# Kernel tuning notes

Measured on AMD Instinct MI355X. Metric: run time of the kernel, lower is better.

## Reference

```python
import jax, jax.numpy as jnp
import numpy as np

B, S, H = 1, 1024, 2880
NQ, NKV, D = 64, 8, 64          # query heads, kv heads, head_dim
G = NQ // NKV                    # GQA group size
W = 128                          # sliding window
SCALE = D ** -0.5
NEG = -1e30


def rotate_half(x):
    x1, x2 = jnp.split(x, 2, axis=-1)
    return jnp.concatenate((-x2, x1), axis=-1)


def setup_inputs() -> dict:
    key = jax.random.key(0)
    ks = jax.random.split(key, 8)
    hidden_states = jax.random.normal(ks[0], (B, S, H), jnp.float32)
    # rotary tables, half head_dim (module concats (cos,cos) to full dim)
    pos = jnp.arange(S, dtype=jnp.float32)[:, None]
    inv = 1.0 / (10000.0 ** (jnp.arange(0, D, 2, dtype=jnp.float32) / D))
    ang = pos * inv[None, :]                      # (S, D/2)
    cos = jnp.cos(ang)[None].astype(jnp.float32)  # (1, S, D/2)
    sin = jnp.sin(ang)[None].astype(jnp.float32)
    w_qkv = jax.random.normal(ks[1], (H, (NQ + 2 * NKV) * D), jnp.float32) * 0.02
    b_qkv = jax.random.normal(ks[2], ((NQ + 2 * NKV) * D,), jnp.float32) * 0.02
    w_o = jax.random.normal(ks[3], (NQ * D, H), jnp.float32) * 0.02
    b_o = jax.random.normal(ks[4], (H,), jnp.float32) * 0.02
    sinks = jax.random.normal(ks[5], (NQ,), jnp.float32)
    k_cache = jnp.zeros((B, S, NKV, D), jnp.float32)
    v_cache = jnp.zeros((B, S, NKV, D), jnp.float32)
    return {"hidden_states": hidden_states, "cos": cos, "sin": sin,
            "w_qkv": w_qkv, "b_qkv": b_qkv, "w_o": w_o, "b_o": b_o,
            "sinks": sinks, "k_cache": k_cache, "v_cache": v_cache, "kv_len": 0}


def reference(hidden_states, cos, sin, w_qkv, b_qkv, w_o, b_o, sinks,
              k_cache, v_cache, kv_len):
    # fused QKV projection + split
    qkv = hidden_states @ w_qkv + b_qkv                      # (B, S, (NQ+2*NKV)*D)
    q, k, v = jnp.split(qkv, [NQ * D, NQ * D + NKV * D], axis=-1)
    q = q.reshape(B, S, NQ, D)
    k = k.reshape(B, S, NKV, D)
    v = v.reshape(B, S, NKV, D)
    # RoPE (BSND layout, half-dim tables duplicated to full dim)
    cosf = jnp.concatenate((cos, cos), axis=-1)[:, :, None, :]
    sinf = jnp.concatenate((sin, sin), axis=-1)[:, :, None, :]
    q = q * cosf + rotate_half(q) * sinf
    k = k * cosf + rotate_half(k) * sinf
    # KV-cache scatter update at position kv_len along seq dim
    k_cache = jax.lax.dynamic_update_slice(k_cache, k, (0, kv_len, 0, 0))
    v_cache = jax.lax.dynamic_update_slice(v_cache, v, (0, kv_len, 0, 0))
    T = kv_len + S
    keys = k_cache[:, :T]                                    # (B, T, NKV, D)
    vals = v_cache[:, :T]
    # GQA: group query heads by kv head
    qg = q.reshape(B, S, NKV, G, D)
    scores = jnp.einsum('bqhgd,bkhd->bhgqk', qg, keys) * SCALE  # (B,NKV,G,S,T)
    # causal + sliding-window mask
    i = jnp.arange(S)[:, None] + kv_len
    j = jnp.arange(T)[None, :]
    allowed = (j <= i) & (i - j < W)
    scores = jnp.where(allowed, scores, NEG)
    # softmax with per-head learnable sink logit (sink gets no value)
    sk = sinks.reshape(NKV, G)[None, :, :, None]             # (1,NKV,G,1)
    m = jnp.maximum(jnp.max(scores, axis=-1), sk)            # (B,NKV,G,S)
    p = jnp.exp(scores - m[..., None])
    denom = jnp.sum(p, axis=-1) + jnp.exp(sk - m)
    attn = jnp.einsum('bhgqk,bkhd->bqhgd', p / denom[..., None], vals)
    out = attn.reshape(B, S, NQ * D) @ w_o + b_o             # (B, S, H)
    return out
```

## Files before the change

kernel.cpp:

```cpp
#include <hip/hip_runtime.h>
#include <hip/hip_bf16.h>

#define NQH 64
#define NKVH 8
#define DH 64
#define SEQ 1024
#define HID 2880
#define QKV_N 5120
#define ATTN_N 4096
#define WIN 128
#define WO_NPAD 2944
#define SCALE_F 0.125f

typedef __attribute__((ext_vector_type(8))) __bf16 bf16x8;
typedef __attribute__((ext_vector_type(4))) float f32x4;

#define GLOAD_LDS16(g, l) \
    __builtin_amdgcn_global_load_lds((const __attribute__((address_space(1))) void*)(g), \
                                     (__attribute__((address_space(3))) void*)(l), 16, 0, 0)

__device__ __forceinline__ ushort f2bf(float x) {
    union { float f; unsigned int u; } c; c.f = x;
    unsigned int u = c.u;
    unsigned int r = (u + 0x7FFFu + ((u >> 16) & 1u)) >> 16;
    return (ushort)r;
}

__global__ __launch_bounds__(256) void convert_f32_bf16(
    const float* __restrict__ in, ushort* __restrict__ out, int n4)
{
    int idx = blockIdx.x * blockDim.x + threadIdx.x;
    int stride = gridDim.x * blockDim.x;
    for (int i = idx; i < n4; i += stride) {
        float4 v = reinterpret_cast<const float4*>(in)[i];
        ushort4 o;
        o.x = f2bf(v.x); o.y = f2bf(v.y); o.z = f2bf(v.z); o.w = f2bf(v.w);
        reinterpret_cast<ushort4*>(out)[i] = o;
    }
}

__global__ __launch_bounds__(256) void transpose_convert(
    const float* __restrict__ in, ushort* __restrict__ out, int K, int N)
{
    __shared__ ushort tile[64][80];
    const int bk = blockIdx.x * 64;
    const int bn = blockIdx.y * 64;
    const int tid = threadIdx.x;
    const bool inb = bn < N;

#pragma unroll
    for (int it = 0; it < 4; ++it) {
        int r = it * 16 + (tid >> 4);
        int c4 = (tid & 15) * 4;
        float4 v = make_float4(0.f, 0.f, 0.f, 0.f);
        if (inb) v = *(const float4*)&in[(size_t)(bk + r) * N + bn + c4];
        tile[c4 + 0][r] = f2bf(v.x);
        tile[c4 + 1][r] = f2bf(v.y);
        tile[c4 + 2][r] = f2bf(v.z);
        tile[c4 + 3][r] = f2bf(v.w);
    }
    __syncthreads();
#pragma unroll
    for (int it = 0; it < 2; ++it) {
        int nr = it * 32 + (tid >> 3);
        int c8 = (tid & 7) * 8;
        uint4 v = *(const uint4*)&tile[nr][c8];
        *(uint4*)&out[(size_t)(bn + nr) * K + bk + c8] = v;
    }
}

template<bool ROPE>
__global__ __launch_bounds__(256) void gemm64x128(
    const ushort* __restrict__ A, const ushort* __restrict__ BT,
    const float* __restrict__ bias, float* __restrict__ C,
    int K, int ldC, int Nreal,
    const float* __restrict__ cosp, const float* __restrict__ sinp)
{
    __shared__ ushort Al[2 * 64 * 64];
    __shared__ ushort Bl[2 * 128 * 64];
    const int t = threadIdx.x;
    const int lane = t & 63;
    const int w = t >> 6;
    const int wr = w >> 1, wc = w & 1;
    const int g4 = lane >> 4;
    const int r15 = lane & 15;

    const int flat = blockIdx.x + gridDim.x * blockIdx.y;
    const int per = (gridDim.x * gridDim.y) >> 3;
    const int virt = (flat & 7) * per + (flat >> 3);
    const int m0 = (virt & 15) * 64;
    const int n0 = (virt >> 4) * 128;

    const ushort* aSrc0; const ushort* aSrc1;
    ushort* aDst0; ushort* aDst1;
    {
        int lin0 = t, lin1 = 256 + t;
        int row0 = lin0 >> 3, row1 = lin1 >> 3;
        int ch0 = (lin0 & 7) ^ (row0 & 7);
        int ch1 = (lin1 & 7) ^ (row1 & 7);
        aSrc0 = A + (size_t)(m0 + row0) * K + ch0 * 8;
        aSrc1 = A + (size_t)(m0 + row1) * K + ch1 * 8;
        aDst0 = &Al[lin0 * 8];
        aDst1 = &Al[lin1 * 8];
    }
    const ushort* bSrc0; const ushort* bSrc1; const ushort* bSrc2; const ushort* bSrc3;
    ushort* bDst0; ushort* bDst1; ushort* bDst2; ushort* bDst3;
    {
        int lin;
        lin = t;       bSrc0 = BT + (size_t)(n0 + (lin >> 3)) * K + (((lin & 7) ^ ((lin >> 3) & 7)) * 8); bDst0 = &Bl[lin * 8];
        lin = 256 + t; bSrc1 = BT + (size_t)(n0 + (lin >> 3)) * K + (((lin & 7) ^ ((lin >> 3) & 7)) * 8); bDst1 = &Bl[lin * 8];
        lin = 512 + t; bSrc2 = BT + (size_t)(n0 + (lin >> 3)) * K + (((lin & 7) ^ ((lin >> 3) & 7)) * 8); bDst2 = &Bl[lin * 8];
        lin = 768 + t; bSrc3 = BT + (size_t)(n0 + (lin >> 3)) * K + (((lin & 7) ^ ((lin >> 3) & 7)) * 8); bDst3 = &Bl[lin * 8];
    }

#define STAGE_TILE(bufsel) do { \
        GLOAD_LDS16(aSrc0, aDst0 + (bufsel) * 4096); \
        GLOAD_LDS16(aSrc1, aDst1 + (bufsel) * 4096); \
        GLOAD_LDS16(bSrc0, bDst0 + (bufsel) * 8192); \
        GLOAD_LDS16(bSrc1, bDst1 + (bufsel) * 8192); \
        GLOAD_LDS16(bSrc2, bDst2 + (bufsel) * 8192); \
        GLOAD_LDS16(bSrc3, bDst3 + (bufsel) * 8192); \
        aSrc0 += 64; aSrc1 += 64; \
        bSrc0 += 64; bSrc1 += 64; bSrc2 += 64; bSrc3 += 64; \
    } while (0)

    int aoff[2][2], boff[4][2];
#pragma unroll
    for (int mi = 0; mi < 2; ++mi)
#pragma unroll
        for (int ks = 0; ks < 2; ++ks) {
            int row = wr * 32 + mi * 16 + r15;
            int slot = (ks * 4 + g4) ^ (row & 7);
            aoff[mi][ks] = row * 64 + slot * 8;
        }
#pragma unroll
    for (int ni = 0; ni < 4; ++ni)
#pragma unroll
        for (int ks = 0; ks < 2; ++ks) {
            int col = wc * 64 + ni * 16 + r15;
            int slot = (ks * 4 + g4) ^ (col & 7);
            boff[ni][ks] = col * 64 + slot * 8;
        }

    f32x4 acc[2][4];
#pragma unroll
    for (int mi = 0; mi < 2; ++mi)
#pragma unroll
        for (int ni = 0; ni < 4; ++ni) acc[mi][ni] = (f32x4){0.f, 0.f, 0.f, 0.f};

#define COMPUTE_TILE(bufsel) do { \
        const ushort* Ab = &Al[(bufsel) * 4096]; \
        const ushort* Bb = &Bl[(bufsel) * 8192]; \
        _Pragma("unroll") \
        for (int ks = 0; ks < 2; ++ks) { \
            bf16x8 a0 = *(const bf16x8*)&Ab[aoff[0][ks]]; \
            bf16x8 a1 = *(const bf16x8*)&Ab[aoff[1][ks]]; \
            bf16x8 b0 = *(const bf16x8*)&Bb[boff[0][ks]]; \
            bf16x8 b1 = *(const bf16x8*)&Bb[boff[1][ks]]; \
            bf16x8 b2 = *(const bf16x8*)&Bb[boff[2][ks]]; \
            bf16x8 b3 = *(const bf16x8*)&Bb[boff[3][ks]]; \
            acc[0][0] = __builtin_amdgcn_mfma_f32_16x16x32_bf16(a0, b0, acc[0][0], 0, 0, 0); \
            acc[0][1] = __builtin_amdgcn_mfma_f32_16x16x32_bf16(a0, b1, acc[0][1], 0, 0, 0); \
            acc[0][2] = __builtin_amdgcn_mfma_f32_16x16x32_bf16(a0, b2, acc[0][2], 0, 0, 0); \
            acc[0][3] = __builtin_amdgcn_mfma_f32_16x16x32_bf16(a0, b3, acc[0][3], 0, 0, 0); \
            acc[1][0] = __builtin_amdgcn_mfma_f32_16x16x32_bf16(a1, b0, acc[1][0], 0, 0, 0); \
            acc[1][1] = __builtin_amdgcn_mfma_f32_16x16x32_bf16(a1, b1, acc[1][1], 0, 0, 0); \
            acc[1][2] = __builtin_amdgcn_mfma_f32_16x16x32_bf16(a1, b2, acc[1][2], 0, 0, 0); \
            acc[1][3] = __builtin_amdgcn_mfma_f32_16x16x32_bf16(a1, b3, acc[1][3], 0, 0, 0); \
        } \
    } while (0)

    const int NT = K >> 6;
    STAGE_TILE(0);
    __syncthreads();
    for (int kt = 0; kt < NT; kt += 2) {
        if (kt + 1 < NT) STAGE_TILE(1);
        COMPUTE_TILE(0);
        __syncthreads();
        if (kt + 1 < NT) {
            if (kt + 2 < NT) STAGE_TILE(0);
            COMPUTE_TILE(1);
            __syncthreads();
        }
    }
#undef STAGE_TILE
#undef COMPUTE_TILE

    float vals[2][4][4];
#pragma unroll
    for (int ni = 0; ni < 4; ++ni) {
        int col = n0 + wc * 64 + ni * 16 + r15;
        float bv = (col < Nreal) ? bias[col] : 0.f;
#pragma unroll
        for (int mi = 0; mi < 2; ++mi)
#pragma unroll
            for (int r = 0; r < 4; ++r) vals[mi][ni][r] = acc[mi][ni][r] + bv;
    }
    if (ROPE) {
        const int head = (n0 + wc * 64) >> 6;
        if (head < 72) {
#pragma unroll
            for (int mi = 0; mi < 2; ++mi)
#pragma unroll
                for (int r = 0; r < 4; ++r) {
                    int q = m0 + wr * 32 + mi * 16 + g4 * 4 + r;
#pragma unroll
                    for (int dp = 0; dp < 2; ++dp) {
                        int d = dp * 16 + r15;
                        float c = cosp[q * 32 + d];
                        float s = sinp[q * 32 + d];
                        float x1 = vals[mi][dp][r];
                        float x2 = vals[mi][dp + 2][r];
                        vals[mi][dp][r]     = x1 * c - x2 * s;
                        vals[mi][dp + 2][r] = x2 * c + x1 * s;
                    }
                }
        }
    }
#pragma unroll
    for (int ni = 0; ni < 4; ++ni) {
        int col = n0 + wc * 64 + ni * 16 + r15;
        if (col < Nreal) {
#pragma unroll
            for (int mi = 0; mi < 2; ++mi) {
                int row = m0 + wr * 32 + mi * 16 + g4 * 4;
#pragma unroll
                for (int r = 0; r < 4; ++r)
                    C[(size_t)(row + r) * ldC + col] = vals[mi][ni][r];
            }
        }
    }
}

__global__ __launch_bounds__(512) void attn_mfma_kernel(
    const float* __restrict__ qkv, const float* __restrict__ sinks,
    ushort* __restrict__ attn_out)
{
    __shared__ __align__(16) ushort Kl[160][72];
    __shared__ __align__(16) ushort Vt[64][168];
    __shared__ __align__(16) ushort Pl[8][32][40];
    const int t = threadIdx.x;
    const int w = t >> 6;
    const int l = t & 63;
    const int g4 = l >> 4;
    const int r15 = l & 15;
    const int q0 = blockIdx.x * 32;
    const int hk = blockIdx.y;
    const int kbase = q0 - 128;

#pragma unroll
    for (int i = 0; i < 5; ++i) {
        int idx = i * 512 + t;
        int row = idx >> 4;
        int c4 = (idx & 15) * 4;
        int j = kbase + row;
        float4 kv = make_float4(0.f, 0.f, 0.f, 0.f);
        float4 vv = make_float4(0.f, 0.f, 0.f, 0.f);
        if (j >= 0) {
            kv = *(const float4*)&qkv[(size_t)j * QKV_N + 4096 + hk * 64 + c4];
            vv = *(const float4*)&qkv[(size_t)j * QKV_N + 4608 + hk * 64 + c4];
        }
        ushort4 kp;
        kp.x = f2bf(kv.x); kp.y = f2bf(kv.y); kp.z = f2bf(kv.z); kp.w = f2bf(kv.w);
        *(ushort4*)&Kl[row][c4] = kp;
        Vt[c4 + 0][row] = f2bf(vv.x);
        Vt[c4 + 1][row] = f2bf(vv.y);
        Vt[c4 + 2][row] = f2bf(vv.z);
        Vt[c4 + 3][row] = f2bf(vv.w);
    }

    bf16x8 qf[2][2];
#pragma unroll
    for (int ct = 0; ct < 2; ++ct) {
        int R = w * 32 + ct * 16 + r15;
        int q = q0 + (R & 31);
        int hq = hk * 8 + (R >> 5);
        const float* qb = &qkv[(size_t)q * QKV_N + hq * 64];
#pragma unroll
        for (int s = 0; s < 2; ++s) {
            float4 a = *(const float4*)&qb[s * 32 + g4 * 8];
            float4 b = *(const float4*)&qb[s * 32 + g4 * 8 + 4];
            union { ushort u[8]; bf16x8 v; } pk;
            pk.u[0] = f2bf(a.x * SCALE_F); pk.u[1] = f2bf(a.y * SCALE_F);
            pk.u[2] = f2bf(a.z * SCALE_F); pk.u[3] = f2bf(a.w * SCALE_F);
            pk.u[4] = f2bf(b.x * SCALE_F); pk.u[5] = f2bf(b.y * SCALE_F);
            pk.u[6] = f2bf(b.z * SCALE_F); pk.u[7] = f2bf(b.w * SCALE_F);
            qf[ct][s] = pk.v;
        }
    }
    __syncthreads();

    f32x4 sc[10][2];
#pragma unroll
    for (int kt = 0; kt < 10; ++kt) {
        sc[kt][0] = (f32x4){0.f, 0.f, 0.f, 0.f};
        sc[kt][1] = (f32x4){0.f, 0.f, 0.f, 0.f};
    }
#pragma unroll
    for (int kt = 0; kt < 10; ++kt) {
#pragma unroll
        for (int s = 0; s < 2; ++s) {
            bf16x8 kf = *(const bf16x8*)&Kl[kt * 16 + r15][s * 32 + g4 * 8];
            sc[kt][0] = __builtin_amdgcn_mfma_f32_16x16x32_bf16(kf, qf[0][s], sc[kt][0], 0, 0, 0);
            sc[kt][1] = __builtin_amdgcn_mfma_f32_16x16x32_bf16(kf, qf[1][s], sc[kt][1], 0, 0, 0);
        }
    }

    const int minkey = 128 - q0;
#pragma unroll
    for (int ct = 0; ct < 2; ++ct) {
        int R = w * 32 + ct * 16 + r15;
        int ql = R & 31;
        float snk = sinks[hk * 8 + (R >> 5)];
#pragma unroll
        for (int kt = 0; kt < 10; ++kt)
#pragma unroll
            for (int r = 0; r < 4; ++r) {
                int key = kt * 16 + g4 * 4 + r;
                bool ok = (key > ql) && (key <= ql + 128) && (key >= minkey);
                if (!ok) sc[kt][ct][r] = -1e30f;
            }
        float m = snk;
#pragma unroll
        for (int kt = 0; kt < 10; ++kt)
#pragma unroll
            for (int r = 0; r < 4; ++r) m = fmaxf(m, sc[kt][ct][r]);
        m = fmaxf(m, __shfl_xor(m, 16));
        m = fmaxf(m, __shfl_xor(m, 32));
        float sum = 0.f;
#pragma unroll
        for (int kt = 0; kt < 10; ++kt)
#pragma unroll
            for (int r = 0; r < 4; ++r) {
                float p = __expf(sc[kt][ct][r] - m);
                sc[kt][ct][r] = p;
                sum += p;
            }
        sum += __shfl_xor(sum, 16);
        sum += __shfl_xor(sum, 32);
        sum += __expf(snk - m);
        float iv = 1.0f / sum;
#pragma unroll
        for (int kt = 0; kt < 10; ++kt)
#pragma unroll
            for (int r = 0; r < 4; ++r) sc[kt][ct][r] *= iv;
    }

    f32x4 pv[2][4];
#pragma unroll
    for (int mi = 0; mi < 2; ++mi)
#pragma unroll
        for (int ni = 0; ni < 4; ++ni) pv[mi][ni] = (f32x4){0.f, 0.f, 0.f, 0.f};

#pragma unroll
    for (int s = 0; s < 5; ++s) {
#pragma unroll
        for (int ct = 0; ct < 2; ++ct)
#pragma unroll
            for (int kh = 0; kh < 2; ++kh) {
                int kt = 2 * s + kh;
                ushort4 p4;
                p4.x = f2bf(sc[kt][ct][0]);
                p4.y = f2bf(sc[kt][ct][1]);
                p4.z = f2bf(sc[kt][ct][2]);
                p4.w = f2bf(sc[kt][ct][3]);
                *(ushort4*)&Pl[w][ct * 16 + r15][kh * 16 + g4 * 4] = p4;
            }
#pragma unroll
        for (int mi = 0; mi < 2; ++mi) {
            bf16x8 pf = *(const bf16x8*)&Pl[w][mi * 16 + r15][g4 * 8];
#pragma unroll
            for (int ni = 0; ni < 4; ++ni) {
                bf16x8 vf = *(const bf16x8*)&Vt[ni * 16 + r15][s * 32 + g4 * 8];
                pv[mi][ni] = __builtin_amdgcn_mfma_f32_16x16x32_bf16(pf, vf, pv[mi][ni], 0, 0, 0);
            }
        }
    }

#pragma unroll
    for (int mi = 0; mi < 2; ++mi)
#pragma unroll
        for (int r = 0; r < 4; ++r) {
            int R = w * 32 + mi * 16 + g4 * 4 + r;
            int q = q0 + (R & 31);
            int hq = hk * 8 + (R >> 5);
            ushort* ob = &attn_out[(size_t)q * ATTN_N + hq * 64 + r15];
#pragma unroll
            for (int ni = 0; ni < 4; ++ni)
                ob[ni * 16] = f2bf(pv[mi][ni][r]);
        }
}

extern "C" void kernel_launch(void* const* d_in, const int* in_sizes, int n_in,
                              void* d_out, int out_size, void* d_ws, size_t ws_size,
                              hipStream_t stream)
{
    const float* hidden = (const float*)d_in[0];
    const float* cosp   = (const float*)d_in[1];
    const float* sinp   = (const float*)d_in[2];
    const float* w_qkv  = (const float*)d_in[3];
    const float* b_qkv  = (const float*)d_in[4];
    const float* w_o    = (const float*)d_in[5];
    const float* b_o    = (const float*)d_in[6];
    const float* sinks  = (const float*)d_in[7];

    char* ws = (char*)d_ws;
    size_t off = 0;
    ushort* wqkvT = (ushort*)(ws + off); off += (size_t)QKV_N * HID * 2;
    ushort* woT   = (ushort*)(ws + off); off += (size_t)WO_NPAD * ATTN_N * 2;
    float*  qkv   = (float*)(ws + off);  off += (size_t)SEQ * QKV_N * 4;
    ushort* hidden_b = (ushort*)(ws + off);
    ushort* attn_b   = (ushort*)(ws + off); off += (size_t)SEQ * ATTN_N * 2;
    if (off > ws_size) return;

    transpose_convert<<<dim3(HID / 64, QKV_N / 64), 256, 0, stream>>>(w_qkv, wqkvT, HID, QKV_N);
    transpose_convert<<<dim3(ATTN_N / 64, WO_NPAD / 64), 256, 0, stream>>>(w_o, woT, ATTN_N, HID);
    convert_f32_bf16<<<2048, 256, 0, stream>>>(hidden, hidden_b, SEQ * HID / 4);

    gemm64x128<true><<<dim3(QKV_N / 128, SEQ / 64), 256, 0, stream>>>(
        hidden_b, wqkvT, b_qkv, qkv, HID, QKV_N, QKV_N, cosp, sinp);

    attn_mfma_kernel<<<dim3(SEQ / 32, NKVH), 512, 0, stream>>>(qkv, sinks, attn_b);

    gemm64x128<false><<<dim3(WO_NPAD / 128, SEQ / 64), 256, 0, stream>>>(
        attn_b, woT, b_o, (float*)d_out, ATTN_N, HID, HID, nullptr, nullptr);
}
```

Before: 147.9 us.

## Shrink GEMM tiles to 64x64 with triple-buffered LDS pipeline and MFMA priority

Replaces the 64x128 GEMM tile with a 64x64 tile, where each wave computes 16 rows by 64 columns. The grid doubles, which gives better occupancy and wave balance across CUs. The double-buffered LDS pipeline becomes a three-stage ring, with explicit vmcnt waits and raw s_barrier so that two tiles of global loads stay in flight. MFMA groups are also wrapped in s_setprio. The cost is less data reuse per block, more global/L2 traffic for the B operand, and reliance on exact vmcnt accounting.

```diff
diff --git a/kernel.cpp b/kernel.cpp
--- a/kernel.cpp
+++ b/kernel.cpp
@@ -70,18 +70,17 @@
 }
 
 template<bool ROPE>
-__global__ __launch_bounds__(256) void gemm64x128(
+__global__ __launch_bounds__(256) void gemm64x64(
     const ushort* __restrict__ A, const ushort* __restrict__ BT,
     const float* __restrict__ bias, float* __restrict__ C,
     int K, int ldC, int Nreal,
     const float* __restrict__ cosp, const float* __restrict__ sinp)
 {
-    __shared__ ushort Al[2 * 64 * 64];
-    __shared__ ushort Bl[2 * 128 * 64];
+    __shared__ ushort Al[3 * 4096];
+    __shared__ ushort Bl[3 * 4096];
     const int t = threadIdx.x;
     const int lane = t & 63;
     const int w = t >> 6;
-    const int wr = w >> 1, wc = w & 1;
     const int g4 = lane >> 4;
     const int r15 = lane & 15;
 
@@ -89,145 +88,124 @@
     const int per = (gridDim.x * gridDim.y) >> 3;
     const int virt = (flat & 7) * per + (flat >> 3);
     const int m0 = (virt & 15) * 64;
-    const int n0 = (virt >> 4) * 128;
-
-    const ushort* aSrc0; const ushort* aSrc1;
-    ushort* aDst0; ushort* aDst1;
+    const int n0 = (virt >> 4) * 64;
+
+    const ushort *aS0, *aS1, *bS0, *bS1;
+    int aO0, aO1;
     {
         int lin0 = t, lin1 = 256 + t;
         int row0 = lin0 >> 3, row1 = lin1 >> 3;
-        int ch0 = (lin0 & 7) ^ (row0 & 7);
-        int ch1 = (lin1 & 7) ^ (row1 & 7);
-        aSrc0 = A + (size_t)(m0 + row0) * K + ch0 * 8;
-        aSrc1 = A + (size_t)(m0 + row1) * K + ch1 * 8;
-        aDst0 = &Al[lin0 * 8];
-        aDst1 = &Al[lin1 * 8];
-    }
-    const ushort* bSrc0; const ushort* bSrc1; const ushort* bSrc2; const ushort* bSrc3;
-    ushort* bDst0; ushort* bDst1; ushort* bDst2; ushort* bDst3;
-    {
-        int lin;
-        lin = t;       bSrc0 = BT + (size_t)(n0 + (lin >> 3)) * K + (((lin & 7) ^ ((lin >> 3) & 7)) * 8); bDst0 = &Bl[lin * 8];
-        lin = 256 + t; bSrc1 = BT + (size_t)(n0 + (lin >> 3)) * K + (((lin & 7) ^ ((lin >> 3) & 7)) * 8); bDst1 = &Bl[lin * 8];
-        lin = 512 + t; bSrc2 = BT + (size_t)(n0 + (lin >> 3)) * K + (((lin & 7) ^ ((lin >> 3) & 7)) * 8); bDst2 = &Bl[lin * 8];
-        lin = 768 + t; bSrc3 = BT + (size_t)(n0 + (lin >> 3)) * K + (((lin & 7) ^ ((lin >> 3) & 7)) * 8); bDst3 = &Bl[lin * 8];
-    }
-
-#define STAGE_TILE(bufsel) do { \
-        GLOAD_LDS16(aSrc0, aDst0 + (bufsel) * 4096); \
-        GLOAD_LDS16(aSrc1, aDst1 + (bufsel) * 4096); \
-        GLOAD_LDS16(bSrc0, bDst0 + (bufsel) * 8192); \
-        GLOAD_LDS16(bSrc1, bDst1 + (bufsel) * 8192); \
-        GLOAD_LDS16(bSrc2, bDst2 + (bufsel) * 8192); \
-        GLOAD_LDS16(bSrc3, bDst3 + (bufsel) * 8192); \
-        aSrc0 += 64; aSrc1 += 64; \
-        bSrc0 += 64; bSrc1 += 64; bSrc2 += 64; bSrc3 += 64; \
+        int sl0 = (lin0 & 7) ^ (row0 & 7);
+        int sl1 = (lin1 & 7) ^ (row1 & 7);
+        aS0 = A  + (size_t)(m0 + row0) * K + sl0 * 8;
+        aS1 = A  + (size_t)(m0 + row1) * K + sl1 * 8;
+        bS0 = BT + (size_t)(n0 + row0) * K + sl0 * 8;
+        bS1 = BT + (size_t)(n0 + row1) * K + sl1 * 8;
+        aO0 = lin0 * 8; aO1 = lin1 * 8;
+    }
+
+#define STAGE_TILE(bi) do { \
+        GLOAD_LDS16(aS0, &Al[(bi) * 4096 + aO0]); \
+        GLOAD_LDS16(aS1, &Al[(bi) * 4096 + aO1]); \
+        GLOAD_LDS16(bS0, &Bl[(bi) * 4096 + aO0]); \
+        GLOAD_LDS16(bS1, &Bl[(bi) * 4096 + aO1]); \
+        aS0 += 64; aS1 += 64; bS0 += 64; bS1 += 64; \
     } while (0)
 
-    int aoff[2][2], boff[4][2];
-#pragma unroll
-    for (int mi = 0; mi < 2; ++mi)
-#pragma unroll
-        for (int ks = 0; ks < 2; ++ks) {
-            int row = wr * 32 + mi * 16 + r15;
-            int slot = (ks * 4 + g4) ^ (row & 7);
-            aoff[mi][ks] = row * 64 + slot * 8;
-        }
-#pragma unroll
-    for (int ni = 0; ni < 4; ++ni)
-#pragma unroll
-        for (int ks = 0; ks < 2; ++ks) {
-            int col = wc * 64 + ni * 16 + r15;
-            int slot = (ks * 4 + g4) ^ (col & 7);
-            boff[ni][ks] = col * 64 + slot * 8;
-        }
-
-    f32x4 acc[2][4];
-#pragma unroll
-    for (int mi = 0; mi < 2; ++mi)
-#pragma unroll
-        for (int ni = 0; ni < 4; ++ni) acc[mi][ni] = (f32x4){0.f, 0.f, 0.f, 0.f};
-
-#define COMPUTE_TILE(bufsel) do { \
-        const ushort* Ab = &Al[(bufsel) * 4096]; \
-        const ushort* Bb = &Bl[(bufsel) * 8192]; \
+    int aoff[2], boff[4][2];
+#pragma unroll
+    for (int ks = 0; ks < 2; ++ks) {
+        int row = w * 16 + r15;
+        aoff[ks] = row * 64 + (((ks * 4 + g4) ^ (row & 7)) * 8);
+#pragma unroll
+        for (int ni = 0; ni < 4; ++ni) {
+            int col = ni * 16 + r15;
+            boff[ni][ks] = col * 64 + (((ks * 4 + g4) ^ (col & 7)) * 8);
+        }
+    }
+
+    f32x4 acc[4];
+#pragma unroll
+    for (int ni = 0; ni < 4; ++ni) acc[ni] = (f32x4){0.f, 0.f, 0.f, 0.f};
+
+#define COMPUTE_TILE(bi) do { \
+        const ushort* Ab = &Al[(bi) * 4096]; \
+        const ushort* Bb = &Bl[(bi) * 4096]; \
         _Pragma("unroll") \
         for (int ks = 0; ks < 2; ++ks) { \
-            bf16x8 a0 = *(const bf16x8*)&Ab[aoff[0][ks]]; \
-            bf16x8 a1 = *(const bf16x8*)&Ab[aoff[1][ks]]; \
+            bf16x8 av = *(const bf16x8*)&Ab[aoff[ks]]; \
             bf16x8 b0 = *(const bf16x8*)&Bb[boff[0][ks]]; \
             bf16x8 b1 = *(const bf16x8*)&Bb[boff[1][ks]]; \
             bf16x8 b2 = *(const bf16x8*)&Bb[boff[2][ks]]; \
             bf16x8 b3 = *(const bf16x8*)&Bb[boff[3][ks]]; \
-            acc[0][0] = __builtin_amdgcn_mfma_f32_16x16x32_bf16(a0, b0, acc[0][0], 0, 0, 0); \
-            acc[0][1] = __builtin_amdgcn_mfma_f32_16x16x32_bf16(a0, b1, acc[0][1], 0, 0, 0); \
-            acc[0][2] = __builtin_amdgcn_mfma_f32_16x16x32_bf16(a0, b2, acc[0][2], 0, 0, 0); \
-            acc[0][3] = __builtin_amdgcn_mfma_f32_16x16x32_bf16(a0, b3, acc[0][3], 0, 0, 0); \
-            acc[1][0] = __builtin_amdgcn_mfma_f32_16x16x32_bf16(a1, b0, acc[1][0], 0, 0, 0); \
-            acc[1][1] = __builtin_amdgcn_mfma_f32_16x16x32_bf16(a1, b1, acc[1][1], 0, 0, 0); \
-            acc[1][2] = __builtin_amdgcn_mfma_f32_16x16x32_bf16(a1, b2, acc[1][2], 0, 0, 0); \
-            acc[1][3] = __builtin_amdgcn_mfma_f32_16x16x32_bf16(a1, b3, acc[1][3], 0, 0, 0); \
+            __builtin_amdgcn_s_setprio(1); \
+            acc[0] = __builtin_amdgcn_mfma_f32_16x16x32_bf16(av, b0, acc[0], 0, 0, 0); \
+            acc[1] = __builtin_amdgcn_mfma_f32_16x16x32_bf16(av, b1, acc[1], 0, 0, 0); \
+            acc[2] = __builtin_amdgcn_mfma_f32_16x16x32_bf16(av, b2, acc[2], 0, 0, 0); \
+            acc[3] = __builtin_amdgcn_mfma_f32_16x16x32_bf16(av, b3, acc[3], 0, 0, 0); \
+            __builtin_amdgcn_s_setprio(0); \
         } \
     } while (0)
 
     const int NT = K >> 6;
     STAGE_TILE(0);
-    __syncthreads();
-    for (int kt = 0; kt < NT; kt += 2) {
-        if (kt + 1 < NT) STAGE_TILE(1);
-        COMPUTE_TILE(0);
-        __syncthreads();
-        if (kt + 1 < NT) {
-            if (kt + 2 < NT) STAGE_TILE(0);
-            COMPUTE_TILE(1);
-            __syncthreads();
-        }
+    STAGE_TILE(1);
+    int bufC = 0, bufS = 2;
+    for (int kt = 0; kt < NT; ++kt) {
+        if (kt + 2 < NT) {
+            STAGE_TILE(bufS);
+            bufS = (bufS == 2) ? 0 : bufS + 1;
+            asm volatile("s_waitcnt vmcnt(8)" ::: "memory");
+        } else if (kt + 2 == NT) {
+            asm volatile("s_waitcnt vmcnt(4)" ::: "memory");
+        } else {
+            asm volatile("s_waitcnt vmcnt(0)" ::: "memory");
+        }
+        __builtin_amdgcn_s_barrier();
+        __builtin_amdgcn_sched_barrier(0);
+        COMPUTE_TILE(bufC);
+        bufC = (bufC == 2) ? 0 : bufC + 1;
+        __builtin_amdgcn_sched_barrier(0);
+        __builtin_amdgcn_s_barrier();
     }
 #undef STAGE_TILE
 #undef COMPUTE_TILE
 
-    float vals[2][4][4];
+    float vals[4][4];
 #pragma unroll
     for (int ni = 0; ni < 4; ++ni) {
-        int col = n0 + wc * 64 + ni * 16 + r15;
+        int col = n0 + ni * 16 + r15;
         float bv = (col < Nreal) ? bias[col] : 0.f;
 #pragma unroll
-        for (int mi = 0; mi < 2; ++mi)
-#pragma unroll
-            for (int r = 0; r < 4; ++r) vals[mi][ni][r] = acc[mi][ni][r] + bv;
+        for (int r = 0; r < 4; ++r) vals[ni][r] = acc[ni][r] + bv;
     }
     if (ROPE) {
-        const int head = (n0 + wc * 64) >> 6;
+        const int head = n0 >> 6;
         if (head < 72) {
 #pragma unroll
-            for (int mi = 0; mi < 2; ++mi)
-#pragma unroll
-                for (int r = 0; r < 4; ++r) {
-                    int q = m0 + wr * 32 + mi * 16 + g4 * 4 + r;
-#pragma unroll
-                    for (int dp = 0; dp < 2; ++dp) {
-                        int d = dp * 16 + r15;
-                        float c = cosp[q * 32 + d];
-                        float s = sinp[q * 32 + d];
-                        float x1 = vals[mi][dp][r];
-                        float x2 = vals[mi][dp + 2][r];
-                        vals[mi][dp][r]     = x1 * c - x2 * s;
-                        vals[mi][dp + 2][r] = x2 * c + x1 * s;
-                    }
+            for (int r = 0; r < 4; ++r) {
+                int q = m0 + w * 16 + g4 * 4 + r;
+#pragma unroll
+                for (int dp = 0; dp < 2; ++dp) {
+                    int d = dp * 16 + r15;
+                    float c = cosp[q * 32 + d];
+                    float s = sinp[q * 32 + d];
+                    float x1 = vals[dp][r];
+                    float x2 = vals[dp + 2][r];
+                    vals[dp][r]     = x1 * c - x2 * s;
+                    vals[dp + 2][r] = x2 * c + x1 * s;
                 }
+            }
         }
     }
 #pragma unroll
     for (int ni = 0; ni < 4; ++ni) {
-        int col = n0 + wc * 64 + ni * 16 + r15;
+        int col = n0 + ni * 16 + r15;
         if (col < Nreal) {
-#pragma unroll
-            for (int mi = 0; mi < 2; ++mi) {
-                int row = m0 + wr * 32 + mi * 16 + g4 * 4;
-#pragma unroll
-                for (int r = 0; r < 4; ++r)
-                    C[(size_t)(row + r) * ldC + col] = vals[mi][ni][r];
-            }
+            int row = m0 + w * 16 + g4 * 4;
+#pragma unroll
+            for (int r = 0; r < 4; ++r)
+                C[(size_t)(row + r) * ldC + col] = vals[ni][r];
         }
     }
 }
@@ -417,11 +395,11 @@
     transpose_convert<<<dim3(ATTN_N / 64, WO_NPAD / 64), 256, 0, stream>>>(w_o, woT, ATTN_N, HID);
     convert_f32_bf16<<<2048, 256, 0, stream>>>(hidden, hidden_b, SEQ * HID / 4);
 
-    gemm64x128<true><<<dim3(QKV_N / 128, SEQ / 64), 256, 0, stream>>>(
+    gemm64x64<true><<<dim3(QKV_N / 64, SEQ / 64), 256, 0, stream>>>(
         hidden_b, wqkvT, b_qkv, qkv, HID, QKV_N, QKV_N, cosp, sinp);
 
     attn_mfma_kernel<<<dim3(SEQ / 32, NKVH), 512, 0, stream>>>(qkv, sinks, attn_b);
 
-    gemm64x128<false><<<dim3(WO_NPAD / 128, SEQ / 64), 256, 0, stream>>>(
+    gemm64x64<false><<<dim3(WO_NPAD / 64, SEQ / 64), 256, 0, stream>>>(
         attn_b, woT, b_o, (float*)d_out, ATTN_N, HID, HID, nullptr, nullptr);
 }
```

Result: slower. 162.3 us (+9.7%).

## Split-K by two for QKV and output GEMMs with separate reduction kernel

Applied to the files above, without the earlier changes.

Both projection GEMMs now split the K dimension in two via blockIdx.z, doubling the block count. Each half writes fp32 partials to a workspace buffer, and a new elementwise kernel sums them. Bias is added only in the first split. RoPE is applied to each partial, which is valid because the rotation is linear. The K tile per stage is halved to 32 with a matching LDS swizzle, which improves wave coverage on the GPU but adds a large partial write/read round trip, two extra launches, and more barriers per unit of work.

```diff
diff --git a/kernel.cpp b/kernel.cpp
--- a/kernel.cpp
+++ b/kernel.cpp
@@ -39,6 +39,20 @@
     }
 }
 
+__global__ __launch_bounds__(256) void reduce_add(
+    const float4* __restrict__ a, const float4* __restrict__ b,
+    float4* __restrict__ o, int n4)
+{
+    int idx = blockIdx.x * blockDim.x + threadIdx.x;
+    int stride = gridDim.x * blockDim.x;
+    for (int i = idx; i < n4; i += stride) {
+        float4 x = a[i], y = b[i];
+        float4 r;
+        r.x = x.x + y.x; r.y = x.y + y.y; r.z = x.z + y.z; r.w = x.w + y.w;
+        o[i] = r;
+    }
+}
+
 __global__ __launch_bounds__(256) void transpose_convert(
     const float* __restrict__ in, ushort* __restrict__ out, int K, int N)
 {
@@ -70,20 +84,21 @@
 }
 
 template<bool ROPE>
-__global__ __launch_bounds__(256) void gemm64x128(
+__global__ __launch_bounds__(256) void gemm_sk(
     const ushort* __restrict__ A, const ushort* __restrict__ BT,
     const float* __restrict__ bias, float* __restrict__ C,
-    int K, int ldC, int Nreal,
+    int Khalf, int Kld, int ldC, int Nreal, size_t cstride,
     const float* __restrict__ cosp, const float* __restrict__ sinp)
 {
-    __shared__ ushort Al[2 * 64 * 64];
-    __shared__ ushort Bl[2 * 128 * 64];
+    __shared__ ushort Al[2 * 2048];
+    __shared__ ushort Bl[2 * 4096];
     const int t = threadIdx.x;
     const int lane = t & 63;
     const int w = t >> 6;
     const int wr = w >> 1, wc = w & 1;
     const int g4 = lane >> 4;
     const int r15 = lane & 15;
+    const int kz = blockIdx.z;
 
     const int flat = blockIdx.x + gridDim.x * blockIdx.y;
     const int per = (gridDim.x * gridDim.y) >> 3;
@@ -91,86 +106,67 @@
     const int m0 = (virt & 15) * 64;
     const int n0 = (virt >> 4) * 128;
 
-    const ushort* aSrc0; const ushort* aSrc1;
-    ushort* aDst0; ushort* aDst1;
+    const ushort *aS, *bS0, *bS1;
+    int aO, bO0, bO1;
     {
+        int rowA = t >> 2;
+        int chA = (t & 3) ^ ((rowA >> 1) & 3);
+        aS = A + (size_t)(m0 + rowA) * Kld + kz * Khalf + chA * 8;
+        aO = t * 8;
         int lin0 = t, lin1 = 256 + t;
-        int row0 = lin0 >> 3, row1 = lin1 >> 3;
-        int ch0 = (lin0 & 7) ^ (row0 & 7);
-        int ch1 = (lin1 & 7) ^ (row1 & 7);
-        aSrc0 = A + (size_t)(m0 + row0) * K + ch0 * 8;
-        aSrc1 = A + (size_t)(m0 + row1) * K + ch1 * 8;
-        aDst0 = &Al[lin0 * 8];
-        aDst1 = &Al[lin1 * 8];
-    }
-    const ushort* bSrc0; const ushort* bSrc1; const ushort* bSrc2; const ushort* bSrc3;
-    ushort* bDst0; ushort* bDst1; ushort* bDst2; ushort* bDst3;
-    {
-        int lin;
-        lin = t;       bSrc0 = BT + (size_t)(n0 + (lin >> 3)) * K + (((lin & 7) ^ ((lin >> 3) & 7)) * 8); bDst0 = &Bl[lin * 8];
-        lin = 256 + t; bSrc1 = BT + (size_t)(n0 + (lin >> 3)) * K + (((lin & 7) ^ ((lin >> 3) & 7)) * 8); bDst1 = &Bl[lin * 8];
-        lin = 512 + t; bSrc2 = BT + (size_t)(n0 + (lin >> 3)) * K + (((lin & 7) ^ ((lin >> 3) & 7)) * 8); bDst2 = &Bl[lin * 8];
-        lin = 768 + t; bSrc3 = BT + (size_t)(n0 + (lin >> 3)) * K + (((lin & 7) ^ ((lin >> 3) & 7)) * 8); bDst3 = &Bl[lin * 8];
-    }
-
-#define STAGE_TILE(bufsel) do { \
-        GLOAD_LDS16(aSrc0, aDst0 + (bufsel) * 4096); \
-        GLOAD_LDS16(aSrc1, aDst1 + (bufsel) * 4096); \
-        GLOAD_LDS16(bSrc0, bDst0 + (bufsel) * 8192); \
-        GLOAD_LDS16(bSrc1, bDst1 + (bufsel) * 8192); \
-        GLOAD_LDS16(bSrc2, bDst2 + (bufsel) * 8192); \
-        GLOAD_LDS16(bSrc3, bDst3 + (bufsel) * 8192); \
-        aSrc0 += 64; aSrc1 += 64; \
-        bSrc0 += 64; bSrc1 += 64; bSrc2 += 64; bSrc3 += 64; \
+        int rowB0 = lin0 >> 2, rowB1 = lin1 >> 2;
+        int chB0 = (lin0 & 3) ^ ((rowB0 >> 1) & 3);
+        int chB1 = (lin1 & 3) ^ ((rowB1 >> 1) & 3);
+        bS0 = BT + (size_t)(n0 + rowB0) * Kld + kz * Khalf + chB0 * 8;
+        bS1 = BT + (size_t)(n0 + rowB1) * Kld + kz * Khalf + chB1 * 8;
+        bO0 = lin0 * 8; bO1 = lin1 * 8;
+    }
+
+#define STAGE_TILE(buf) do { \
+        GLOAD_LDS16(aS,  &Al[(buf) * 2048 + aO]); \
+        GLOAD_LDS16(bS0, &Bl[(buf) * 4096 + bO0]); \
+        GLOAD_LDS16(bS1, &Bl[(buf) * 4096 + bO1]); \
+        aS += 32; bS0 += 32; bS1 += 32; \
     } while (0)
 
-    int aoff[2][2], boff[4][2];
+    int aoff[2], boff[4];
+#pragma unroll
+    for (int mi = 0; mi < 2; ++mi) {
+        int row = wr * 32 + mi * 16 + r15;
+        aoff[mi] = row * 32 + ((g4 ^ ((row >> 1) & 3)) * 8);
+    }
+#pragma unroll
+    for (int ni = 0; ni < 4; ++ni) {
+        int col = wc * 64 + ni * 16 + r15;
+        boff[ni] = col * 32 + ((g4 ^ ((col >> 1) & 3)) * 8);
+    }
+
+    f32x4 acc[2][4];
 #pragma unroll
     for (int mi = 0; mi < 2; ++mi)
 #pragma unroll
-        for (int ks = 0; ks < 2; ++ks) {
-            int row = wr * 32 + mi * 16 + r15;
-            int slot = (ks * 4 + g4) ^ (row & 7);
-            aoff[mi][ks] = row * 64 + slot * 8;
-        }
-#pragma unroll
-    for (int ni = 0; ni < 4; ++ni)
-#pragma unroll
-        for (int ks = 0; ks < 2; ++ks) {
-            int col = wc * 64 + ni * 16 + r15;
-            int slot = (ks * 4 + g4) ^ (col & 7);
-            boff[ni][ks] = col * 64 + slot * 8;
-        }
-
-    f32x4 acc[2][4];
-#pragma unroll
-    for (int mi = 0; mi < 2; ++mi)
-#pragma unroll
         for (int ni = 0; ni < 4; ++ni) acc[mi][ni] = (f32x4){0.f, 0.f, 0.f, 0.f};
 
-#define COMPUTE_TILE(bufsel) do { \
-        const ushort* Ab = &Al[(bufsel) * 4096]; \
-        const ushort* Bb = &Bl[(bufsel) * 8192]; \
-        _Pragma("unroll") \
-        for (int ks = 0; ks < 2; ++ks) { \
-            bf16x8 a0 = *(const bf16x8*)&Ab[aoff[0][ks]]; \
-            bf16x8 a1 = *(const bf16x8*)&Ab[aoff[1][ks]]; \
-            bf16x8 b0 = *(const bf16x8*)&Bb[boff[0][ks]]; \
-            bf16x8 b1 = *(const bf16x8*)&Bb[boff[1][ks]]; \
-            bf16x8 b2 = *(const bf16x8*)&Bb[boff[2][ks]]; \
-            bf16x8 b3 = *(const bf16x8*)&Bb[boff[3][ks]]; \
-            acc[0][0] = __builtin_amdgcn_mfma_f32_16x16x32_bf16(a0, b0, acc[0][0], 0, 0, 0); \
-            acc[0][1] = __builtin_amdgcn_mfma_f32_16x16x32_bf16(a0, b1, acc[0][1], 0, 0, 0); \
-            acc[0][2] = __builtin_amdgcn_mfma_f32_16x16x32_bf16(a0, b2, acc[0][2], 0, 0, 0); \
-            acc[0][3] = __builtin_amdgcn_mfma_f32_16x16x32_bf16(a0, b3, acc[0][3], 0, 0, 0); \
-            acc[1][0] = __builtin_amdgcn_mfma_f32_16x16x32_bf16(a1, b0, acc[1][0], 0, 0, 0); \
-            acc[1][1] = __builtin_amdgcn_mfma_f32_16x16x32_bf16(a1, b1, acc[1][1], 0, 0, 0); \
-            acc[1][2] = __builtin_amdgcn_mfma_f32_16x16x32_bf16(a1, b2, acc[1][2], 0, 0, 0); \
-            acc[1][3] = __builtin_amdgcn_mfma_f32_16x16x32_bf16(a1, b3, acc[1][3], 0, 0, 0); \
-        } \
+#define COMPUTE_TILE(buf) do { \
+        const ushort* Ab = &Al[(buf) * 2048]; \
+        const ushort* Bb = &Bl[(buf) * 4096]; \
+        bf16x8 a0 = *(const bf16x8*)&Ab[aoff[0]]; \
+        bf16x8 a1 = *(const bf16x8*)&Ab[aoff[1]]; \
+        bf16x8 b0 = *(const bf16x8*)&Bb[boff[0]]; \
+        bf16x8 b1 = *(const bf16x8*)&Bb[boff[1]]; \
+        bf16x8 b2 = *(const bf16x8*)&Bb[boff[2]]; \
+        bf16x8 b3 = *(const bf16x8*)&Bb[boff[3]]; \
+        acc[0][0] = __builtin_amdgcn_mfma_f32_16x16x32_bf16(a0, b0, acc[0][0], 0, 0, 0); \
+        acc[0][1] = __builtin_amdgcn_mfma_f32_16x16x32_bf16(a0, b1, acc[0][1], 0, 0, 0); \
+        acc[0][2] = __builtin_amdgcn_mfma_f32_16x16x32_bf16(a0, b2, acc[0][2], 0, 0, 0); \
+        acc[0][3] = __builtin_amdgcn_mfma_f32_16x16x32_bf16(a0, b3, acc[0][3], 0, 0, 0); \
+        acc[1][0] = __builtin_amdgcn_mfma_f32_16x16x32_bf16(a1, b0, acc[1][0], 0, 0, 0); \
+        acc[1][1] = __builtin_amdgcn_mfma_f32_16x16x32_bf16(a1, b1, acc[1][1], 0, 0, 0); \
+        acc[1][2] = __builtin_amdgcn_mfma_f32_16x16x32_bf16(a1, b2, acc[1][2], 0, 0, 0); \
+        acc[1][3] = __builtin_amdgcn_mfma_f32_16x16x32_bf16(a1, b3, acc[1][3], 0, 0, 0); \
     } while (0)
 
-    const int NT = K >> 6;
+    const int NT = Khalf >> 5;
     STAGE_TILE(0);
     __syncthreads();
     for (int kt = 0; kt < NT; kt += 2) {
@@ -190,7 +186,7 @@
 #pragma unroll
     for (int ni = 0; ni < 4; ++ni) {
         int col = n0 + wc * 64 + ni * 16 + r15;
-        float bv = (col < Nreal) ? bias[col] : 0.f;
+        float bv = (kz == 0 && col < Nreal) ? bias[col] : 0.f;
 #pragma unroll
         for (int mi = 0; mi < 2; ++mi)
 #pragma unroll
@@ -217,6 +213,7 @@
                 }
         }
     }
+    float* Cz = C + (size_t)kz * cstride;
 #pragma unroll
     for (int ni = 0; ni < 4; ++ni) {
         int col = n0 + wc * 64 + ni * 16 + r15;
@@ -226,7 +223,7 @@
                 int row = m0 + wr * 32 + mi * 16 + g4 * 4;
 #pragma unroll
                 for (int r = 0; r < 4; ++r)
-                    C[(size_t)(row + r) * ldC + col] = vals[mi][ni][r];
+                    Cz[(size_t)(row + r) * ldC + col] = vals[mi][ni][r];
             }
         }
     }
@@ -411,17 +408,26 @@
     float*  qkv   = (float*)(ws + off);  off += (size_t)SEQ * QKV_N * 4;
     ushort* hidden_b = (ushort*)(ws + off);
     ushort* attn_b   = (ushort*)(ws + off); off += (size_t)SEQ * ATTN_N * 2;
+    float*  part  = (float*)(ws + off);  off += (size_t)2 * SEQ * QKV_N * 4;
     if (off > ws_size) return;
 
     transpose_convert<<<dim3(HID / 64, QKV_N / 64), 256, 0, stream>>>(w_qkv, wqkvT, HID, QKV_N);
     transpose_convert<<<dim3(ATTN_N / 64, WO_NPAD / 64), 256, 0, stream>>>(w_o, woT, ATTN_N, HID);
     convert_f32_bf16<<<2048, 256, 0, stream>>>(hidden, hidden_b, SEQ * HID / 4);
 
-    gemm64x128<true><<<dim3(QKV_N / 128, SEQ / 64), 256, 0, stream>>>(
-        hidden_b, wqkvT, b_qkv, qkv, HID, QKV_N, QKV_N, cosp, sinp);
+    gemm_sk<true><<<dim3(QKV_N / 128, SEQ / 64, 2), 256, 0, stream>>>(
+        hidden_b, wqkvT, b_qkv, part, HID / 2, HID, QKV_N, QKV_N,
+        (size_t)SEQ * QKV_N, cosp, sinp);
+    reduce_add<<<2048, 256, 0, stream>>>(
+        (const float4*)part, (const float4*)(part + (size_t)SEQ * QKV_N),
+        (float4*)qkv, SEQ * QKV_N / 4);
 
     attn_mfma_kernel<<<dim3(SEQ / 32, NKVH), 512, 0, stream>>>(qkv, sinks, attn_b);
 
-    gemm64x128<false><<<dim3(WO_NPAD / 128, SEQ / 64), 256, 0, stream>>>(
-        attn_b, woT, b_o, (float*)d_out, ATTN_N, HID, HID, nullptr, nullptr);
-}
+    gemm_sk<false><<<dim3(WO_NPAD / 128, SEQ / 64, 2), 256, 0, stream>>>(
+        attn_b, woT, b_o, part, ATTN_N / 2, ATTN_N, HID, HID,
+        (size_t)SEQ * HID, nullptr, nullptr);
+    reduce_add<<<2048, 256, 0, stream>>>(
+        (const float4*)part, (const float4*)(part + (size_t)SEQ * HID),
+        (float4*)d_out, SEQ * HID / 4);
+}
```

Result: slower. 173.9 us (+17.5%).

## Enlarge GEMM block tile to 128x128 for both projections

Applied to the files above, without the earlier changes.

Both projection GEMMs now compute a 128x128 output tile per block instead of 64x128. Each wave runs a 4x4 grid of MFMA fragments, and each thread issues four A and four B async loads per k-step. The goal is more data reuse per LDS load and fewer global reads per flop. The cost is half as many blocks, which may leave CUs idle (the output projection has only 184 blocks), plus more LDS and accumulator registers per block.

```diff
diff --git a/kernel.cpp b/kernel.cpp
--- a/kernel.cpp
+++ b/kernel.cpp
@@ -70,14 +70,14 @@
 }
 
 template<bool ROPE>
-__global__ __launch_bounds__(256) void gemm64x128(
+__global__ __launch_bounds__(256) void gemm128sq(
     const ushort* __restrict__ A, const ushort* __restrict__ BT,
     const float* __restrict__ bias, float* __restrict__ C,
     int K, int ldC, int Nreal,
     const float* __restrict__ cosp, const float* __restrict__ sinp)
 {
-    __shared__ ushort Al[2 * 64 * 64];
-    __shared__ ushort Bl[2 * 128 * 64];
+    __shared__ ushort Al[2 * 8192];
+    __shared__ ushort Bl[2 * 8192];
     const int t = threadIdx.x;
     const int lane = t & 63;
     const int w = t >> 6;
@@ -88,85 +88,75 @@
     const int flat = blockIdx.x + gridDim.x * blockIdx.y;
     const int per = (gridDim.x * gridDim.y) >> 3;
     const int virt = (flat & 7) * per + (flat >> 3);
-    const int m0 = (virt & 15) * 64;
-    const int n0 = (virt >> 4) * 128;
-
-    const ushort* aSrc0; const ushort* aSrc1;
-    ushort* aDst0; ushort* aDst1;
-    {
-        int lin0 = t, lin1 = 256 + t;
-        int row0 = lin0 >> 3, row1 = lin1 >> 3;
-        int ch0 = (lin0 & 7) ^ (row0 & 7);
-        int ch1 = (lin1 & 7) ^ (row1 & 7);
-        aSrc0 = A + (size_t)(m0 + row0) * K + ch0 * 8;
-        aSrc1 = A + (size_t)(m0 + row1) * K + ch1 * 8;
-        aDst0 = &Al[lin0 * 8];
-        aDst1 = &Al[lin1 * 8];
-    }
-    const ushort* bSrc0; const ushort* bSrc1; const ushort* bSrc2; const ushort* bSrc3;
-    ushort* bDst0; ushort* bDst1; ushort* bDst2; ushort* bDst3;
-    {
-        int lin;
-        lin = t;       bSrc0 = BT + (size_t)(n0 + (lin >> 3)) * K + (((lin & 7) ^ ((lin >> 3) & 7)) * 8); bDst0 = &Bl[lin * 8];
-        lin = 256 + t; bSrc1 = BT + (size_t)(n0 + (lin >> 3)) * K + (((lin & 7) ^ ((lin >> 3) & 7)) * 8); bDst1 = &Bl[lin * 8];
-        lin = 512 + t; bSrc2 = BT + (size_t)(n0 + (lin >> 3)) * K + (((lin & 7) ^ ((lin >> 3) & 7)) * 8); bDst2 = &Bl[lin * 8];
-        lin = 768 + t; bSrc3 = BT + (size_t)(n0 + (lin >> 3)) * K + (((lin & 7) ^ ((lin >> 3) & 7)) * 8); bDst3 = &Bl[lin * 8];
-    }
-
-#define STAGE_TILE(bufsel) do { \
-        GLOAD_LDS16(aSrc0, aDst0 + (bufsel) * 4096); \
-        GLOAD_LDS16(aSrc1, aDst1 + (bufsel) * 4096); \
-        GLOAD_LDS16(bSrc0, bDst0 + (bufsel) * 8192); \
-        GLOAD_LDS16(bSrc1, bDst1 + (bufsel) * 8192); \
-        GLOAD_LDS16(bSrc2, bDst2 + (bufsel) * 8192); \
-        GLOAD_LDS16(bSrc3, bDst3 + (bufsel) * 8192); \
-        aSrc0 += 64; aSrc1 += 64; \
-        bSrc0 += 64; bSrc1 += 64; bSrc2 += 64; bSrc3 += 64; \
+    const int m0 = (virt & 7) * 128;
+    const int n0 = (virt >> 3) * 128;
+
+    const ushort* aSrc[4]; const ushort* bSrc[4]; int dOff[4];
+#pragma unroll
+    for (int i = 0; i < 4; ++i) {
+        int lin = i * 256 + t;
+        int row = lin >> 3;
+        int ch = (lin & 7) ^ (row & 7);
+        aSrc[i] = A  + (size_t)(m0 + row) * K + ch * 8;
+        bSrc[i] = BT + (size_t)(n0 + row) * K + ch * 8;
+        dOff[i] = lin * 8;
+    }
+
+#define STAGE_TILE(buf) do { \
+        _Pragma("unroll") \
+        for (int i = 0; i < 4; ++i) { \
+            GLOAD_LDS16(aSrc[i], &Al[(buf) * 8192 + dOff[i]]); \
+            GLOAD_LDS16(bSrc[i], &Bl[(buf) * 8192 + dOff[i]]); \
+            aSrc[i] += 64; bSrc[i] += 64; \
+        } \
     } while (0)
 
-    int aoff[2][2], boff[4][2];
-#pragma unroll
-    for (int mi = 0; mi < 2; ++mi)
+    int aoff[4][2], boff[4][2];
+#pragma unroll
+    for (int i = 0; i < 4; ++i)
 #pragma unroll
         for (int ks = 0; ks < 2; ++ks) {
-            int row = wr * 32 + mi * 16 + r15;
-            int slot = (ks * 4 + g4) ^ (row & 7);
-            aoff[mi][ks] = row * 64 + slot * 8;
-        }
-#pragma unroll
-    for (int ni = 0; ni < 4; ++ni)
-#pragma unroll
-        for (int ks = 0; ks < 2; ++ks) {
-            int col = wc * 64 + ni * 16 + r15;
-            int slot = (ks * 4 + g4) ^ (col & 7);
-            boff[ni][ks] = col * 64 + slot * 8;
-        }
-
-    f32x4 acc[2][4];
-#pragma unroll
-    for (int mi = 0; mi < 2; ++mi)
+            int row = wr * 64 + i * 16 + r15;
+            aoff[i][ks] = row * 64 + (((ks * 4 + g4) ^ (row & 7)) * 8);
+            int col = wc * 64 + i * 16 + r15;
+            boff[i][ks] = col * 64 + (((ks * 4 + g4) ^ (col & 7)) * 8);
+        }
+
+    f32x4 acc[4][4];
+#pragma unroll
+    for (int mi = 0; mi < 4; ++mi)
 #pragma unroll
         for (int ni = 0; ni < 4; ++ni) acc[mi][ni] = (f32x4){0.f, 0.f, 0.f, 0.f};
 
-#define COMPUTE_TILE(bufsel) do { \
-        const ushort* Ab = &Al[(bufsel) * 4096]; \
-        const ushort* Bb = &Bl[(bufsel) * 8192]; \
+#define COMPUTE_TILE(buf) do { \
+        const ushort* Ab = &Al[(buf) * 8192]; \
+        const ushort* Bb = &Bl[(buf) * 8192]; \
         _Pragma("unroll") \
         for (int ks = 0; ks < 2; ++ks) { \
-            bf16x8 a0 = *(const bf16x8*)&Ab[aoff[0][ks]]; \
-            bf16x8 a1 = *(const bf16x8*)&Ab[aoff[1][ks]]; \
-            bf16x8 b0 = *(const bf16x8*)&Bb[boff[0][ks]]; \
-            bf16x8 b1 = *(const bf16x8*)&Bb[boff[1][ks]]; \
-            bf16x8 b2 = *(const bf16x8*)&Bb[boff[2][ks]]; \
-            bf16x8 b3 = *(const bf16x8*)&Bb[boff[3][ks]]; \
-            acc[0][0] = __builtin_amdgcn_mfma_f32_16x16x32_bf16(a0, b0, acc[0][0], 0, 0, 0); \
-            acc[0][1] = __builtin_amdgcn_mfma_f32_16x16x32_bf16(a0, b1, acc[0][1], 0, 0, 0); \
-            acc[0][2] = __builtin_amdgcn_mfma_f32_16x16x32_bf16(a0, b2, acc[0][2], 0, 0, 0); \
-            acc[0][3] = __builtin_amdgcn_mfma_f32_16x16x32_bf16(a0, b3, acc[0][3], 0, 0, 0); \
-            acc[1][0] = __builtin_amdgcn_mfma_f32_16x16x32_bf16(a1, b0, acc[1][0], 0, 0, 0); \
-            acc[1][1] = __builtin_amdgcn_mfma_f32_16x16x32_bf16(a1, b1, acc[1][1], 0, 0, 0); \
-            acc[1][2] = __builtin_amdgcn_mfma_f32_16x16x32_bf16(a1, b2, acc[1][2], 0, 0, 0); \
-            acc[1][3] = __builtin_amdgcn_mfma_f32_16x16x32_bf16(a1, b3, acc[1][3], 0, 0, 0); \
+            bf16x8 af0 = *(const bf16x8*)&Ab[aoff[0][ks]]; \
+            bf16x8 af1 = *(const bf16x8*)&Ab[aoff[1][ks]]; \
+            bf16x8 af2 = *(const bf16x8*)&Ab[aoff[2][ks]]; \
+            bf16x8 af3 = *(const bf16x8*)&Ab[aoff[3][ks]]; \
+            bf16x8 bf0 = *(const bf16x8*)&Bb[boff[0][ks]]; \
+            bf16x8 bf1 = *(const bf16x8*)&Bb[boff[1][ks]]; \
+            bf16x8 bf2 = *(const bf16x8*)&Bb[boff[2][ks]]; \
+            bf16x8 bf3 = *(const bf16x8*)&Bb[boff[3][ks]]; \
+            acc[0][0] = __builtin_amdgcn_mfma_f32_16x16x32_bf16(af0, bf0, acc[0][0], 0, 0, 0); \
+            acc[0][1] = __builtin_amdgcn_mfma_f32_16x16x32_bf16(af0, bf1, acc[0][1], 0, 0, 0); \
+            acc[0][2] = __builtin_amdgcn_mfma_f32_16x16x32_bf16(af0, bf2, acc[0][2], 0, 0, 0); \
+            acc[0][3] = __builtin_amdgcn_mfma_f32_16x16x32_bf16(af0, bf3, acc[0][3], 0, 0, 0); \
+            acc[1][0] = __builtin_amdgcn_mfma_f32_16x16x32_bf16(af1, bf0, acc[1][0], 0, 0, 0); \
+            acc[1][1] = __builtin_amdgcn_mfma_f32_16x16x32_bf16(af1, bf1, acc[1][1], 0, 0, 0); \
+            acc[1][2] = __builtin_amdgcn_mfma_f32_16x16x32_bf16(af1, bf2, acc[1][2], 0, 0, 0); \
+            acc[1][3] = __builtin_amdgcn_mfma_f32_16x16x32_bf16(af1, bf3, acc[1][3], 0, 0, 0); \
+            acc[2][0] = __builtin_amdgcn_mfma_f32_16x16x32_bf16(af2, bf0, acc[2][0], 0, 0, 0); \
+            acc[2][1] = __builtin_amdgcn_mfma_f32_16x16x32_bf16(af2, bf1, acc[2][1], 0, 0, 0); \
+            acc[2][2] = __builtin_amdgcn_mfma_f32_16x16x32_bf16(af2, bf2, acc[2][2], 0, 0, 0); \
+            acc[2][3] = __builtin_amdgcn_mfma_f32_16x16x32_bf16(af2, bf3, acc[2][3], 0, 0, 0); \
+            acc[3][0] = __builtin_amdgcn_mfma_f32_16x16x32_bf16(af3, bf0, acc[3][0], 0, 0, 0); \
+            acc[3][1] = __builtin_amdgcn_mfma_f32_16x16x32_bf16(af3, bf1, acc[3][1], 0, 0, 0); \
+            acc[3][2] = __builtin_amdgcn_mfma_f32_16x16x32_bf16(af3, bf2, acc[3][2], 0, 0, 0); \
+            acc[3][3] = __builtin_amdgcn_mfma_f32_16x16x32_bf16(af3, bf3, acc[3][3], 0, 0, 0); \
         } \
     } while (0)
 
@@ -186,33 +176,32 @@
 #undef STAGE_TILE
 #undef COMPUTE_TILE
 
-    float vals[2][4][4];
 #pragma unroll
     for (int ni = 0; ni < 4; ++ni) {
         int col = n0 + wc * 64 + ni * 16 + r15;
         float bv = (col < Nreal) ? bias[col] : 0.f;
 #pragma unroll
-        for (int mi = 0; mi < 2; ++mi)
-#pragma unroll
-            for (int r = 0; r < 4; ++r) vals[mi][ni][r] = acc[mi][ni][r] + bv;
+        for (int mi = 0; mi < 4; ++mi)
+#pragma unroll
+            for (int r = 0; r < 4; ++r) acc[mi][ni][r] += bv;
     }
     if (ROPE) {
         const int head = (n0 + wc * 64) >> 6;
         if (head < 72) {
 #pragma unroll
-            for (int mi = 0; mi < 2; ++mi)
+            for (int mi = 0; mi < 4; ++mi)
 #pragma unroll
                 for (int r = 0; r < 4; ++r) {
-                    int q = m0 + wr * 32 + mi * 16 + g4 * 4 + r;
+                    int q = m0 + wr * 64 + mi * 16 + g4 * 4 + r;
 #pragma unroll
                     for (int dp = 0; dp < 2; ++dp) {
                         int d = dp * 16 + r15;
                         float c = cosp[q * 32 + d];
                         float s = sinp[q * 32 + d];
-                        float x1 = vals[mi][dp][r];
-                        float x2 = vals[mi][dp + 2][r];
-                        vals[mi][dp][r]     = x1 * c - x2 * s;
-                        vals[mi][dp + 2][r] = x2 * c + x1 * s;
+                        float x1 = acc[mi][dp][r];
+                        float x2 = acc[mi][dp + 2][r];
+                        acc[mi][dp][r]     = x1 * c - x2 * s;
+                        acc[mi][dp + 2][r] = x2 * c + x1 * s;
                     }
                 }
         }
@@ -222,11 +211,11 @@
         int col = n0 + wc * 64 + ni * 16 + r15;
         if (col < Nreal) {
 #pragma unroll
-            for (int mi = 0; mi < 2; ++mi) {
-                int row = m0 + wr * 32 + mi * 16 + g4 * 4;
+            for (int mi = 0; mi < 4; ++mi) {
+                int row = m0 + wr * 64 + mi * 16 + g4 * 4;
 #pragma unroll
                 for (int r = 0; r < 4; ++r)
-                    C[(size_t)(row + r) * ldC + col] = vals[mi][ni][r];
+                    C[(size_t)(row + r) * ldC + col] = acc[mi][ni][r];
             }
         }
     }
@@ -417,11 +406,11 @@
     transpose_convert<<<dim3(ATTN_N / 64, WO_NPAD / 64), 256, 0, stream>>>(w_o, woT, ATTN_N, HID);
     convert_f32_bf16<<<2048, 256, 0, stream>>>(hidden, hidden_b, SEQ * HID / 4);
 
-    gemm64x128<true><<<dim3(QKV_N / 128, SEQ / 64), 256, 0, stream>>>(
+    gemm128sq<true><<<dim3(QKV_N / 128, SEQ / 128), 256, 0, stream>>>(
         hidden_b, wqkvT, b_qkv, qkv, HID, QKV_N, QKV_N, cosp, sinp);
 
     attn_mfma_kernel<<<dim3(SEQ / 32, NKVH), 512, 0, stream>>>(qkv, sinks, attn_b);
 
-    gemm64x128<false><<<dim3(WO_NPAD / 128, SEQ / 64), 256, 0, stream>>>(
+    gemm128sq<false><<<dim3(WO_NPAD / 128, SEQ / 128), 256, 0, stream>>>(
         attn_b, woT, b_o, (float*)d_out, ATTN_N, HID, HID, nullptr, nullptr);
 }
```

Measured after the change: 162.8 us. 1.1x slower.
